# Kernel tuning notes

Hardware: AMD Instinct MI355X
Metric: run time of the kernel (lower is better)

Reference implementation:

```python
import jax, jax.numpy as jnp
import numpy as np

S, B, C = 7, 2, 80
LAMBDA_COORDS = 5.0
LAMBDA_NOOBJ = 0.5


def _iou_cxcywh(a, b):
    """Elementwise IoU of boxes in cx,cy,w,h format, shapes (..., 4) -> (...).
    Same math as torchvision box_convert(cxcywh->xyxy) + box_iou diagonal,
    computed directly (O(S^2)) instead of the O(S^4) pairwise matrix."""
    ax1 = a[..., 0] - a[..., 2] * 0.5
    ay1 = a[..., 1] - a[..., 3] * 0.5
    ax2 = a[..., 0] + a[..., 2] * 0.5
    ay2 = a[..., 1] + a[..., 3] * 0.5
    bx1 = b[..., 0] - b[..., 2] * 0.5
    by1 = b[..., 1] - b[..., 3] * 0.5
    bx2 = b[..., 0] + b[..., 2] * 0.5
    by2 = b[..., 1] + b[..., 3] * 0.5
    inter_w = jnp.clip(jnp.minimum(ax2, bx2) - jnp.maximum(ax1, bx1), 0.0)
    inter_h = jnp.clip(jnp.minimum(ay2, by2) - jnp.maximum(ay1, by1), 0.0)
    inter = inter_w * inter_h
    area_a = (ax2 - ax1) * (ay2 - ay1)
    area_b = (bx2 - bx1) * (by2 - by1)
    return inter / (area_a + area_b - inter)


def setup_inputs() -> dict:
    key = jax.random.key(0)
    k1, k2 = jax.random.split(key)
    N = 8192
    predictions = jax.random.normal(k1, (N, S, S, C + 5 * B), dtype=jnp.float32)
    target = jax.random.uniform(k2, (N, S, S, C + 5), dtype=jnp.float32)
    return {"predictions": predictions, "target": target}


def reference(predictions, target):
    preds = predictions.reshape(-1, S, S, C + 5 * B)
    target_boxes = target[..., -4:]                 # (N,S,S,4)
    pred_boxes_1 = preds[..., -4:]
    pred_boxes_2 = preds[..., -9:-5]

    iou1 = _iou_cxcywh(pred_boxes_1, target_boxes)  # (N,S,S) == diag of box_iou
    iou2 = _iou_cxcywh(pred_boxes_2, target_boxes)
    ious_idx = jnp.argmax(jnp.stack([iou1, iou2], axis=0), axis=0)  # (N,S,S)

    m1 = (1 - ious_idx).astype(preds.dtype)  # responsible-box masks
    m2 = ious_idx.astype(preds.dtype)
    obj = target[..., -5]                    # objectness (N,S,S)

    pred_boxes = obj[..., None] * (m1[..., None] * pred_boxes_1 + m2[..., None] * pred_boxes_2)

    dims = jnp.sign(pred_boxes[..., -2:]) * jnp.sqrt(jnp.abs(pred_boxes[..., -2:]) + 1e-6)
    target_dims = jnp.sqrt(target_boxes[..., -2:])

    sse = lambda a, b: jnp.sum((a - b) ** 2)  # MSELoss(reduction='sum')

    center_loss = sse(pred_boxes[..., :-3], target_boxes[..., :-3]) * LAMBDA_COORDS
    dimensions_loss = sse(dims, target_dims) * LAMBDA_COORDS
    coords_loss = center_loss + dimensions_loss

    obj_pred = preds[..., -5] * m1 + preds[..., -10] * m2
    obj_loss = sse(obj * obj_pred, obj)
    noobj_loss = sse((1.0 - obj) * obj_pred, obj) * LAMBDA_NOOBJ

    classes_loss = sse(preds[..., :-10] * obj[..., None], target[..., :-5])

    return (coords_loss, obj_loss, noobj_loss, classes_loss)
```

## Files before the change

### kernel.cpp

```cpp
#include <hip/hip_runtime.h>


#define NPRED 90
#define NTGT  85
#define NCLS  80
#define CHUNK 64
#define TPB   256
#define PBS   11
#define NBLK  1536

#define NT4 (CHUNK * NTGT / 4)
#define NP4 (CHUNK * NPRED / 4)

__device__ __forceinline__ float sgnf(float x) {
    return (x > 0.0f) ? 1.0f : ((x < 0.0f) ? -1.0f : 0.0f);
}

__device__ __forceinline__ float iou_vs_target(
    float acx, float acy, float aw, float ah,
    float bx1, float by1, float bx2, float by2, float area_b)
{
    float ax1 = acx - aw * 0.5f, ay1 = acy - ah * 0.5f;
    float ax2 = acx + aw * 0.5f, ay2 = acy + ah * 0.5f;
    float iw = fmaxf(fminf(ax2, bx2) - fmaxf(ax1, bx1), 0.0f);
    float ih = fmaxf(fminf(ay2, by2) - fmaxf(ay1, by1), 0.0f);
    float inter = iw * ih;
    float area_a = (ax2 - ax1) * (ay2 - ay1);
    return inter / (area_a + area_b - inter);
}

__device__ __forceinline__ void proc_elem(float v, int cl, int j, float obj,
    const float* __restrict__ t_lds, float* __restrict__ pbox, float& clsl)
{
    if (j < NCLS) {
        float tv = t_lds[cl * NTGT + j];
        float d = fmaf(v, obj, -tv);
        clsl = fmaf(d, d, clsl);
    } else {
        pbox[cl * PBS + (j - NCLS)] = v;
    }
}

__device__ __forceinline__ void proc_quad(float4 v, int q,
    const float* __restrict__ t_lds, float* __restrict__ pbox, float& clsl)
{
    int f  = 4 * q;
    int cl = f / NPRED;
    int j  = f - cl * NPRED;
    if (j != 88) {
        float obj = t_lds[cl * NTGT + NCLS];
        proc_elem(v.x, cl, j,     obj, t_lds, pbox, clsl);
        proc_elem(v.y, cl, j + 1, obj, t_lds, pbox, clsl);
        proc_elem(v.z, cl, j + 2, obj, t_lds, pbox, clsl);
        proc_elem(v.w, cl, j + 3, obj, t_lds, pbox, clsl);
    } else {
        pbox[cl * PBS + 8] = v.x;
        pbox[cl * PBS + 9] = v.y;
        float obj2 = t_lds[(cl + 1) * NTGT + NCLS];
        proc_elem(v.z, cl + 1, 0, obj2, t_lds, pbox, clsl);
        proc_elem(v.w, cl + 1, 1, obj2, t_lds, pbox, clsl);
    }
}

__global__ __launch_bounds__(TPB) void yolo_loss_kernel(
    const float* __restrict__ preds, const float* __restrict__ targ,
    float* __restrict__ part, float* __restrict__ out,
    int n_cells, int mode)
{
    __shared__ __align__(16) float t_lds[CHUNK * NTGT];
    __shared__ float pbox[CHUNK * PBS];
    __shared__ float red[4][4];

    float coords = 0.0f, objl = 0.0f, noobjl = 0.0f, clsl = 0.0f;

    const int tid = threadIdx.x;
    const int n_chunks = n_cells / CHUNK;

    for (int ch = blockIdx.x; ch < n_chunks; ch += gridDim.x) {
        const float4* tg4 = (const float4*)(targ  + (size_t)ch * (CHUNK * NTGT));
        const float4* pr4 = (const float4*)(preds + (size_t)ch * (CHUNK * NPRED));

        float4 t0 = tg4[tid];
        float4 t1 = tg4[tid + 256];
        float4 t2 = tg4[tid + 512];
        float4 t3 = tg4[tid + 768];
        float4 t4 = tg4[tid + 1024];
        const bool ht = tid < (NT4 - 1280);
        float4 t5 = make_float4(0.f, 0.f, 0.f, 0.f);
        if (ht) t5 = tg4[tid + 1280];

        float4 p0 = pr4[tid];
        float4 p1 = pr4[tid + 256];
        float4 p2 = pr4[tid + 512];
        float4 p3 = pr4[tid + 768];
        float4 p4 = pr4[tid + 1024];
        const bool hp = tid < (NP4 - 1280);
        float4 p5 = make_float4(0.f, 0.f, 0.f, 0.f);
        if (hp) p5 = pr4[tid + 1280];

        __syncthreads();

        float4* tl4 = (float4*)t_lds;
        tl4[tid]        = t0;
        tl4[tid + 256]  = t1;
        tl4[tid + 512]  = t2;
        tl4[tid + 768]  = t3;
        tl4[tid + 1024] = t4;
        if (ht) tl4[tid + 1280] = t5;

        __syncthreads();

        proc_quad(p0, tid,        t_lds, pbox, clsl);
        proc_quad(p1, tid + 256,  t_lds, pbox, clsl);
        proc_quad(p2, tid + 512,  t_lds, pbox, clsl);
        proc_quad(p3, tid + 768,  t_lds, pbox, clsl);
        proc_quad(p4, tid + 1024, t_lds, pbox, clsl);
        if (hp) proc_quad(p5, tid + 1280, t_lds, pbox, clsl);

        __syncthreads();

        if (tid < CHUNK) {
            const float* pb = &pbox[tid * PBS];
            const float* tc = &t_lds[tid * NTGT + NCLS];
            float obj = tc[0];
            float tcx = tc[1], tcy = tc[2], tw = tc[3], th = tc[4];
            float bx1 = tcx - tw * 0.5f, by1 = tcy - th * 0.5f;
            float bx2 = tcx + tw * 0.5f, by2 = tcy + th * 0.5f;
            float area_b = (bx2 - bx1) * (by2 - by1);

            float iou1 = iou_vs_target(pb[6], pb[7], pb[8], pb[9],
                                       bx1, by1, bx2, by2, area_b);
            float iou2 = iou_vs_target(pb[1], pb[2], pb[3], pb[4],
                                       bx1, by1, bx2, by2, area_b);
            bool use2 = iou2 > iou1;

            float pcx = obj * (use2 ? pb[1] : pb[6]);
            float pw  = obj * (use2 ? pb[3] : pb[8]);
            float ph  = obj * (use2 ? pb[4] : pb[9]);

            float dc = pcx - tcx;
            float dw = sgnf(pw) * sqrtf(fabsf(pw) + 1e-6f) - sqrtf(tw);
            float dh = sgnf(ph) * sqrtf(fabsf(ph) + 1e-6f) - sqrtf(th);
            coords = fmaf(dc, dc, coords);
            coords = fmaf(dw, dw, coords);
            coords = fmaf(dh, dh, coords);

            float obj_pred = use2 ? pb[0] : pb[5];
            float e1 = fmaf(obj, obj_pred, -obj);
            objl = fmaf(e1, e1, objl);
            float e2 = fmaf(1.0f - obj, obj_pred, -obj);
            noobjl = fmaf(e2, e2, noobjl);
        }
    }

    for (int cell = n_chunks * CHUNK + (int)(blockIdx.x * TPB + tid);
         cell < n_cells; cell += gridDim.x * TPB) {
        const float* p = preds + (size_t)cell * NPRED;
        const float* t = targ  + (size_t)cell * NTGT;
        float obj = t[NCLS];
        float cls = 0.0f;
        for (int k = 0; k < NCLS; ++k) {
            float d = fmaf(p[k], obj, -t[k]);
            cls = fmaf(d, d, cls);
        }
        clsl += cls;
        float tcx = t[81], tcy = t[82], tw = t[83], th = t[84];
        float bx1 = tcx - tw * 0.5f, by1 = tcy - th * 0.5f;
        float bx2 = tcx + tw * 0.5f, by2 = tcy + th * 0.5f;
        float area_b = (bx2 - bx1) * (by2 - by1);
        float iou1 = iou_vs_target(p[86], p[87], p[88], p[89],
                                   bx1, by1, bx2, by2, area_b);
        float iou2 = iou_vs_target(p[81], p[82], p[83], p[84],
                                   bx1, by1, bx2, by2, area_b);
        bool use2 = iou2 > iou1;
        float pcx = obj * (use2 ? p[81] : p[86]);
        float pw  = obj * (use2 ? p[83] : p[88]);
        float ph  = obj * (use2 ? p[84] : p[89]);
        float dc = pcx - tcx;
        float dw = sgnf(pw) * sqrtf(fabsf(pw) + 1e-6f) - sqrtf(tw);
        float dh = sgnf(ph) * sqrtf(fabsf(ph) + 1e-6f) - sqrtf(th);
        coords = fmaf(dc, dc, coords);
        coords = fmaf(dw, dw, coords);
        coords = fmaf(dh, dh, coords);
        float obj_pred = use2 ? p[80] : p[85];
        float e1 = fmaf(obj, obj_pred, -obj);
        objl = fmaf(e1, e1, objl);
        float e2 = fmaf(1.0f - obj, obj_pred, -obj);
        noobjl = fmaf(e2, e2, noobjl);
    }

    #pragma unroll
    for (int off = 32; off > 0; off >>= 1) {
        coords += __shfl_down(coords, off);
        objl   += __shfl_down(objl, off);
        noobjl += __shfl_down(noobjl, off);
        clsl   += __shfl_down(clsl, off);
    }

    int wave = threadIdx.x >> 6;
    int lane = threadIdx.x & 63;
    __syncthreads();
    if (lane == 0) {
        red[0][wave] = coords;
        red[1][wave] = objl;
        red[2][wave] = noobjl;
        red[3][wave] = clsl;
    }
    __syncthreads();
    if (threadIdx.x == 0) {
        float c = red[0][0] + red[0][1] + red[0][2] + red[0][3];
        float o = red[1][0] + red[1][1] + red[1][2] + red[1][3];
        float n = red[2][0] + red[2][1] + red[2][2] + red[2][3];
        float k = red[3][0] + red[3][1] + red[3][2] + red[3][3];
        if (mode == 0) {
            int nb = gridDim.x;
            part[0 * nb + blockIdx.x] = c;
            part[1 * nb + blockIdx.x] = o;
            part[2 * nb + blockIdx.x] = n;
            part[3 * nb + blockIdx.x] = k;
        } else {
            atomicAdd(&out[0], 5.0f * c);
            atomicAdd(&out[1], o);
            atomicAdd(&out[2], 0.5f * n);
            atomicAdd(&out[3], k);
        }
    }
}

__global__ __launch_bounds__(256) void yolo_reduce_kernel(
    const float* __restrict__ part, float* __restrict__ out, int nblk)
{
    int w = threadIdx.x >> 6;
    int lane = threadIdx.x & 63;
    float s = 0.0f;
    for (int i = lane; i < nblk; i += 64) s += part[w * nblk + i];
    #pragma unroll
    for (int off = 32; off > 0; off >>= 1) s += __shfl_down(s, off);
    if (lane == 0) {
        float scale = (w == 0) ? 5.0f : (w == 2) ? 0.5f : 1.0f;
        out[w] = s * scale;
    }
}

extern "C" void kernel_launch(void* const* d_in, const int* in_sizes, int n_in,
                              void* d_out, int out_size, void* d_ws, size_t ws_size,
                              hipStream_t stream) {
    const float* preds = (const float*)d_in[0];
    const float* targ  = (const float*)d_in[1];
    float* out = (float*)d_out;

    int n_cells = in_sizes[0] / NPRED;

    bool use_ws = ws_size >= (size_t)(4 * NBLK) * sizeof(float);

    if (use_ws) {
        float* part = (float*)d_ws;
        hipLaunchKernelGGL(yolo_loss_kernel, dim3(NBLK), dim3(TPB), 0, stream,
                           preds, targ, part, out, n_cells, 0);
        hipLaunchKernelGGL(yolo_reduce_kernel, dim3(1), dim3(256), 0, stream,
                           part, out, NBLK);
        if (out_size > 4) {
            hipMemsetAsync(out + 4, 0, (size_t)(out_size - 4) * sizeof(float), stream);
        }
    } else {
        hipMemsetAsync(d_out, 0, (size_t)out_size * sizeof(float), stream);
        hipLaunchKernelGGL(yolo_loss_kernel, dim3(NBLK), dim3(TPB), 0, stream,
                           preds, targ, (float*)nullptr, out, n_cells, 1);
    }
}
```

Before: 299.1 us.

## Double-buffer chunks via direct global-to-LDS async loads with contiguous block ranges

```diff
diff --git a/kernel.cpp b/kernel.cpp
--- a/kernel.cpp
+++ b/kernel.cpp
@@ -1,16 +1,29 @@
 #include <hip/hip_runtime.h>
+#include <stdint.h>
 
 
 #define NPRED 90
 #define NTGT  85
 #define NCLS  80
-#define CHUNK 64
+#define CHUNK 32
 #define TPB   256
-#define PBS   11
-#define NBLK  1536
+#define NBLK  768
 
 #define NT4 (CHUNK * NTGT / 4)
 #define NP4 (CHUNK * NPRED / 4)
+
+#define WAITVM6() asm volatile("s_waitcnt vmcnt(6)" ::: "memory")
+#define WAITVM0() asm volatile("s_waitcnt vmcnt(0)" ::: "memory")
+#define BARRIER() do { __builtin_amdgcn_sched_barrier(0); \
+                       __builtin_amdgcn_s_barrier();      \
+                       __builtin_amdgcn_sched_barrier(0); } while (0)
+
+__device__ __forceinline__ void load_lds16(const float4* g, float4* l) {
+    __builtin_amdgcn_global_load_lds(
+        (const __attribute__((address_space(1))) void*)g,
+        (__attribute__((address_space(3))) void*)l,
+        16, 0, 0);
+}
 
 __device__ __forceinline__ float sgnf(float x) {
     return (x > 0.0f) ? 1.0f : ((x < 0.0f) ? -1.0f : 0.0f);
@@ -29,36 +42,52 @@
     return inter / (area_a + area_b - inter);
 }
 
-__device__ __forceinline__ void proc_elem(float v, int cl, int j, float obj,
-    const float* __restrict__ t_lds, float* __restrict__ pbox, float& clsl)
+__device__ __forceinline__ void pe(float v, int cl, int j, float obj,
+                                   const float* __restrict__ tl, float& clsl)
 {
     if (j < NCLS) {
-        float tv = t_lds[cl * NTGT + j];
-        float d = fmaf(v, obj, -tv);
+        float d = fmaf(v, obj, -tl[cl * NTGT + j]);
         clsl = fmaf(d, d, clsl);
-    } else {
-        pbox[cl * PBS + (j - NCLS)] = v;
     }
 }
 
 __device__ __forceinline__ void proc_quad(float4 v, int q,
-    const float* __restrict__ t_lds, float* __restrict__ pbox, float& clsl)
+    const float* __restrict__ tl, float& clsl)
 {
     int f  = 4 * q;
     int cl = f / NPRED;
     int j  = f - cl * NPRED;
     if (j != 88) {
-        float obj = t_lds[cl * NTGT + NCLS];
-        proc_elem(v.x, cl, j,     obj, t_lds, pbox, clsl);
-        proc_elem(v.y, cl, j + 1, obj, t_lds, pbox, clsl);
-        proc_elem(v.z, cl, j + 2, obj, t_lds, pbox, clsl);
-        proc_elem(v.w, cl, j + 3, obj, t_lds, pbox, clsl);
+        float obj = tl[cl * NTGT + NCLS];
+        pe(v.x, cl, j,     obj, tl, clsl);
+        pe(v.y, cl, j + 1, obj, tl, clsl);
+        pe(v.z, cl, j + 2, obj, tl, clsl);
+        pe(v.w, cl, j + 3, obj, tl, clsl);
     } else {
-        pbox[cl * PBS + 8] = v.x;
-        pbox[cl * PBS + 9] = v.y;
-        float obj2 = t_lds[(cl + 1) * NTGT + NCLS];
-        proc_elem(v.z, cl + 1, 0, obj2, t_lds, pbox, clsl);
-        proc_elem(v.w, cl + 1, 1, obj2, t_lds, pbox, clsl);
+        float obj2 = tl[(cl + 1) * NTGT + NCLS];
+        pe(v.z, cl + 1, 0, obj2, tl, clsl);
+        pe(v.w, cl + 1, 1, obj2, tl, clsl);
+    }
+}
+
+__device__ __forceinline__ void stage_chunk(
+    const float4* __restrict__ tg, const float4* __restrict__ pg,
+    float4* tb, float4* pb, int wave, int lane)
+{
+    if (wave < 2) {
+        #pragma unroll
+        for (int s = 0; s < 6; ++s) {
+            int base = (wave + 2 * s) * 64;
+            if (base > NT4 - 64) base = NT4 - 64;
+            load_lds16(tg + base + lane, tb + base);
+        }
+    } else {
+        #pragma unroll
+        for (int s = 0; s < 6; ++s) {
+            int base = ((wave - 2) + 2 * s) * 64;
+            if (base > NP4 - 64) base = NP4 - 64;
+            load_lds16(pg + base + lane, pb + base);
+        }
     }
 }
 
@@ -67,89 +96,80 @@
     float* __restrict__ part, float* __restrict__ out,
     int n_cells, int mode)
 {
-    __shared__ __align__(16) float t_lds[CHUNK * NTGT];
-    __shared__ float pbox[CHUNK * PBS];
+    __shared__ float4 tbuf[2][NT4];
+    __shared__ float4 pbuf[2][NP4];
     __shared__ float red[4][4];
 
     float coords = 0.0f, objl = 0.0f, noobjl = 0.0f, clsl = 0.0f;
 
-    const int tid = threadIdx.x;
+    const int tid  = threadIdx.x;
+    const int wave = tid >> 6;
+    const int lane = tid & 63;
     const int n_chunks = n_cells / CHUNK;
 
-    for (int ch = blockIdx.x; ch < n_chunks; ch += gridDim.x) {
-        const float4* tg4 = (const float4*)(targ  + (size_t)ch * (CHUNK * NTGT));
-        const float4* pr4 = (const float4*)(preds + (size_t)ch * (CHUNK * NPRED));
-
-        float4 t0 = tg4[tid];
-        float4 t1 = tg4[tid + 256];
-        float4 t2 = tg4[tid + 512];
-        float4 t3 = tg4[tid + 768];
-        float4 t4 = tg4[tid + 1024];
-        const bool ht = tid < (NT4 - 1280);
-        float4 t5 = make_float4(0.f, 0.f, 0.f, 0.f);
-        if (ht) t5 = tg4[tid + 1280];
-
-        float4 p0 = pr4[tid];
-        float4 p1 = pr4[tid + 256];
-        float4 p2 = pr4[tid + 512];
-        float4 p3 = pr4[tid + 768];
-        float4 p4 = pr4[tid + 1024];
-        const bool hp = tid < (NP4 - 1280);
-        float4 p5 = make_float4(0.f, 0.f, 0.f, 0.f);
-        if (hp) p5 = pr4[tid + 1280];
-
-        __syncthreads();
-
-        float4* tl4 = (float4*)t_lds;
-        tl4[tid]        = t0;
-        tl4[tid + 256]  = t1;
-        tl4[tid + 512]  = t2;
-        tl4[tid + 768]  = t3;
-        tl4[tid + 1024] = t4;
-        if (ht) tl4[tid + 1280] = t5;
-
-        __syncthreads();
-
-        proc_quad(p0, tid,        t_lds, pbox, clsl);
-        proc_quad(p1, tid + 256,  t_lds, pbox, clsl);
-        proc_quad(p2, tid + 512,  t_lds, pbox, clsl);
-        proc_quad(p3, tid + 768,  t_lds, pbox, clsl);
-        proc_quad(p4, tid + 1024, t_lds, pbox, clsl);
-        if (hp) proc_quad(p5, tid + 1280, t_lds, pbox, clsl);
-
-        __syncthreads();
-
-        if (tid < CHUNK) {
-            const float* pb = &pbox[tid * PBS];
-            const float* tc = &t_lds[tid * NTGT + NCLS];
-            float obj = tc[0];
-            float tcx = tc[1], tcy = tc[2], tw = tc[3], th = tc[4];
-            float bx1 = tcx - tw * 0.5f, by1 = tcy - th * 0.5f;
-            float bx2 = tcx + tw * 0.5f, by2 = tcy + th * 0.5f;
-            float area_b = (bx2 - bx1) * (by2 - by1);
-
-            float iou1 = iou_vs_target(pb[6], pb[7], pb[8], pb[9],
-                                       bx1, by1, bx2, by2, area_b);
-            float iou2 = iou_vs_target(pb[1], pb[2], pb[3], pb[4],
-                                       bx1, by1, bx2, by2, area_b);
-            bool use2 = iou2 > iou1;
-
-            float pcx = obj * (use2 ? pb[1] : pb[6]);
-            float pw  = obj * (use2 ? pb[3] : pb[8]);
-            float ph  = obj * (use2 ? pb[4] : pb[9]);
-
-            float dc = pcx - tcx;
-            float dw = sgnf(pw) * sqrtf(fabsf(pw) + 1e-6f) - sqrtf(tw);
-            float dh = sgnf(ph) * sqrtf(fabsf(ph) + 1e-6f) - sqrtf(th);
-            coords = fmaf(dc, dc, coords);
-            coords = fmaf(dw, dw, coords);
-            coords = fmaf(dh, dh, coords);
-
-            float obj_pred = use2 ? pb[0] : pb[5];
-            float e1 = fmaf(obj, obj_pred, -obj);
-            objl = fmaf(e1, e1, objl);
-            float e2 = fmaf(1.0f - obj, obj_pred, -obj);
-            noobjl = fmaf(e2, e2, noobjl);
+    const int start = (int)(((long long)blockIdx.x       * n_chunks) / gridDim.x);
+    const int end   = (int)(((long long)(blockIdx.x + 1) * n_chunks) / gridDim.x);
+
+    if (start < end) {
+        int cur = 0;
+        stage_chunk((const float4*)(targ  + (size_t)start * (CHUNK * NTGT)),
+                    (const float4*)(preds + (size_t)start * (CHUNK * NPRED)),
+                    tbuf[0], pbuf[0], wave, lane);
+
+        for (int ch = start; ch < end; ++ch) {
+            if (ch + 1 < end) {
+                stage_chunk((const float4*)(targ  + (size_t)(ch + 1) * (CHUNK * NTGT)),
+                            (const float4*)(preds + (size_t)(ch + 1) * (CHUNK * NPRED)),
+                            tbuf[cur ^ 1], pbuf[cur ^ 1], wave, lane);
+                WAITVM6();
+            } else {
+                WAITVM0();
+            }
+            BARRIER();
+
+            const float* tl = (const float*)&tbuf[cur][0];
+            const float* pl = (const float*)&pbuf[cur][0];
+
+            proc_quad(pbuf[cur][tid],       tid,       tl, clsl);
+            proc_quad(pbuf[cur][tid + 256], tid + 256, tl, clsl);
+            if (tid < NP4 - 512)
+                proc_quad(pbuf[cur][tid + 512], tid + 512, tl, clsl);
+
+            if (tid < CHUNK) {
+                const float* pb = pl + tid * NPRED + NCLS;
+                const float* tc = tl + tid * NTGT + NCLS;
+                float obj = tc[0];
+                float tcx = tc[1], tcy = tc[2], tw = tc[3], th = tc[4];
+                float bx1 = tcx - tw * 0.5f, by1 = tcy - th * 0.5f;
+                float bx2 = tcx + tw * 0.5f, by2 = tcy + th * 0.5f;
+                float area_b = (bx2 - bx1) * (by2 - by1);
+
+                float iou1 = iou_vs_target(pb[6], pb[7], pb[8], pb[9],
+                                           bx1, by1, bx2, by2, area_b);
+                float iou2 = iou_vs_target(pb[1], pb[2], pb[3], pb[4],
+                                           bx1, by1, bx2, by2, area_b);
+                bool use2 = iou2 > iou1;
+
+                float pcx = obj * (use2 ? pb[1] : pb[6]);
+                float pw  = obj * (use2 ? pb[3] : pb[8]);
+                float ph  = obj * (use2 ? pb[4] : pb[9]);
+
+                float dc = pcx - tcx;
+                float dw = sgnf(pw) * sqrtf(fabsf(pw) + 1e-6f) - sqrtf(tw);
+                float dh = sgnf(ph) * sqrtf(fabsf(ph) + 1e-6f) - sqrtf(th);
+                coords = fmaf(dc, dc, coords);
+                coords = fmaf(dw, dw, coords);
+                coords = fmaf(dh, dh, coords);
+
+                float obj_pred = use2 ? pb[0] : pb[5];
+                float e1 = fmaf(obj, obj_pred, -obj);
+                objl = fmaf(e1, e1, objl);
+                float e2 = fmaf(1.0f - obj, obj_pred, -obj);
+                noobjl = fmaf(e2, e2, noobjl);
+            }
+
+            BARRIER();
+            cur ^= 1;
         }
     }
 
@@ -197,8 +217,6 @@
         clsl   += __shfl_down(clsl, off);
     }
 
-    int wave = threadIdx.x >> 6;
-    int lane = threadIdx.x & 63;
     __syncthreads();
     if (lane == 0) {
         red[0][wave] = coords;
@@ -207,7 +225,7 @@
         red[3][wave] = clsl;
     }
     __syncthreads();
-    if (threadIdx.x == 0) {
+    if (tid == 0) {
         float c = red[0][0] + red[0][1] + red[0][2] + red[0][3];
         float o = red[1][0] + red[1][1] + red[1][2] + red[1][3];
         float n = red[2][0] + red[2][1] + red[2][2] + red[2][3];
```

New measurement: 302.0 us. No clear change (+1.0%).
